# Optimization experiments

Hardware: AMD Instinct MI355X
Metric: run time of the kernel (lower is better)

## Reference

```python
import jax, jax.numpy as jnp
import numpy as np

N_NODES = 100000


def _gcn_norm(edge_index, num_nodes):
    # PyG GCNConv default: add self-loops, symmetric normalization.
    src = jnp.concatenate([edge_index[0], jnp.arange(num_nodes, dtype=edge_index.dtype)])
    dst = jnp.concatenate([edge_index[1], jnp.arange(num_nodes, dtype=edge_index.dtype)])
    deg = jax.ops.segment_sum(jnp.ones_like(dst, dtype=jnp.float32), dst, num_segments=num_nodes)
    dis = jnp.where(deg > 0, jax.lax.rsqrt(deg), 0.0)  # deg^{-1/2}
    norm = dis[src] * dis[dst]  # [E + N]
    return src, dst, norm


def _gcn_conv(x, W, b, src, dst, norm, num_nodes):
    h = x @ W.T                      # [N, out] transform first (out < in)
    msg = h[src] * norm[:, None]     # gather + per-edge scale
    agg = jax.ops.segment_sum(msg, dst, num_segments=num_nodes)  # scatter-add
    return agg + b


def setup_inputs() -> dict:
    key = jax.random.key(0)
    ks = jax.random.split(key, 12)
    E = 3200000
    x = jax.random.normal(ks[0], (N_NODES, 128), dtype=jnp.float32)
    edge_index = jax.random.randint(ks[1], (2, E), 0, N_NODES, dtype=jnp.int64)
    s = lambda k, sh, fan: jax.random.normal(k, sh, dtype=jnp.float32) * (1.0 / np.sqrt(fan))
    return {
        "x": x,
        "edge_index": edge_index,
        "W1": s(ks[2], (32, 128), 128), "b1": jnp.zeros((32,), jnp.float32),
        "W2": s(ks[3], (16, 32), 32),   "b2": jnp.zeros((16,), jnp.float32),
        "w_ih": s(ks[4], (32, 16), 16), "w_hh": s(ks[5], (32, 8), 8),
        "b_ih": s(ks[6], (32,), 8),     "b_hh": s(ks[7], (32,), 8),
        "W_out": s(ks[8], (1, 8), 8),   "b_out": jnp.zeros((1,), jnp.float32),
    }


def reference(x, edge_index, W1, b1, W2, b2, w_ih, w_hh, b_ih, b_hh, W_out, b_out):
    src, dst, norm = _gcn_norm(edge_index, N_NODES)
    h = jax.nn.relu(_gcn_conv(x, W1, b1, src, dst, norm, N_NODES))   # [N, 32]
    h = jax.nn.relu(_gcn_conv(h, W2, b2, src, dst, norm, N_NODES))   # [N, 16]
    # Single-timestep LSTM with h0 = c0 = 0 (gate order: i, f, g, o).
    gates = h @ w_ih.T + b_ih + b_hh   # [N, 32]; h0 @ w_hh.T term is zero
    i, f, g, o = jnp.split(gates, 4, axis=-1)
    c = jax.nn.sigmoid(i) * jnp.tanh(g)
    hh = jax.nn.sigmoid(o) * jnp.tanh(c)  # [N, 8]
    out = hh @ W_out.T + b_out            # [N, 1]
    return out.squeeze(-1)                # [N]
```

## Files before the change

### kernel.cpp

```cpp
#include <hip/hip_runtime.h>
#include <hip/hip_fp16.h>
#include <math.h>

static constexpr int N = 100000;
static constexpr int SHIFT = 7;
static constexpr int BUCKN = 1 << SHIFT;
static constexpr int NBUCK = (N + BUCKN - 1) >> SHIFT;
static constexpr int CHUNK = 12288;
static constexpr int STRIDE = 5120;

__global__ __launch_bounds__(1024) void k_init(int* __restrict__ gcur) {
    int b = threadIdx.x;
    if (b < NBUCK) gcur[b] = b * STRIDE;
}

__global__ __launch_bounds__(1024) void k_part(const int* __restrict__ src,
                                               const int* __restrict__ dst,
                                               int* __restrict__ gcur,
                                               int* __restrict__ col, int E) {
    __shared__ int ss[CHUNK];
    __shared__ int ds[CHUNK];
    __shared__ int hl[NBUCK];
    __shared__ int cur[NBUCK];
    const int t = threadIdx.x, b = blockIdx.x;
    if (t < NBUCK) hl[t] = 0;
    __syncthreads();
    const int e0 = b * CHUNK;
    const int m = min(CHUNK, E - e0);
    for (int i = t; i < m; i += 1024) {
        int d = dst[e0 + i], s = src[e0 + i];
        ss[i] = s;
        ds[i] = d;
        atomicAdd(&hl[d >> SHIFT], 1);
    }
    __syncthreads();
    if (t < NBUCK) cur[t] = atomicAdd(&gcur[t], hl[t]);
    __syncthreads();
    for (int i = t; i < m; i += 1024) {
        int d = ds[i];
        int pos = atomicAdd(&cur[d >> SHIFT], 1);
        col[pos] = ss[i] | ((d & (BUCKN - 1)) << 17);
    }
}

__global__ __launch_bounds__(1024) void k_sort(const int* __restrict__ gcur,
                                               int* __restrict__ col,
                                               int* __restrict__ deg,
                                               int* __restrict__ row_start) {
    __shared__ int es[STRIDE];
    __shared__ int cnt[BUCKN];
    __shared__ int cur[BUCKN];
    const int t = threadIdx.x, buck = blockIdx.x;
    const int s0 = buck * STRIDE;
    int n = gcur[buck] - s0;
    if (n > STRIDE) n = STRIDE;
    if (t < BUCKN) cnt[t] = 0;
    __syncthreads();
    for (int i = t; i < n; i += 1024) {
        int p = col[s0 + i];
        es[i] = p;
        atomicAdd(&cnt[(p >> 17) & (BUCKN - 1)], 1);
    }
    __syncthreads();
    if (t < BUCKN) cur[t] = cnt[t];
    __syncthreads();
    for (int off = 1; off < BUCKN; off <<= 1) {
        int v = (t < BUCKN && t >= off) ? cur[t - off] : 0;
        __syncthreads();
        if (t < BUCKN) cur[t] += v;
        __syncthreads();
    }
    if (t < BUCKN) {
        int excl = cur[t] - cnt[t];
        int node = buck * BUCKN + t;
        if (node < N) {
            deg[node] = cnt[t];
            row_start[node] = s0 + excl;
        }
        cur[t] = excl;
    }
    __syncthreads();
    for (int i = t; i < n; i += 1024) {
        int p = es[i];
        int pos = atomicAdd(&cur[(p >> 17) & (BUCKN - 1)], 1);
        col[s0 + pos] = p & 0x1FFFF;
    }
}

__global__ __launch_bounds__(256) void k_xw1(
        const float* __restrict__ x, const float* __restrict__ W1,
        const int* __restrict__ deg, __half* __restrict__ g1h) {
    __shared__ float wt[128 * 33];
    __shared__ float xs[8 * 128];
    const int t = threadIdx.x;
    for (int idx = t; idx < 4096; idx += 256) {
        int j = idx >> 7, k = idx & 127;
        wt[k * 33 + j] = W1[idx];
    }
    const float4* x4 = (const float4*)x + (size_t)blockIdx.x * 256;
    ((float4*)xs)[t] = x4[t];
    __syncthreads();

    const int nl = t >> 5, j = t & 31;
    const int node = blockIdx.x * 8 + nl;
    const float* xr = xs + nl * 128;
    float a = 0.f;
#pragma unroll 8
    for (int k = 0; k < 128; ++k) a = fmaf(xr[k], wt[k * 33 + j], a);
    g1h[blockIdx.x * 256 + t] = __float2half(a * rsqrtf((float)(deg[node] + 1)));
}

__global__ __launch_bounds__(256) void k_gather1(
        const int* __restrict__ row_start, const int* __restrict__ deg,
        const int* __restrict__ col, const __half* __restrict__ g1h,
        const float* __restrict__ b1, float* __restrict__ h1) {
    const int t = threadIdx.x;
    const int node = blockIdx.x * 8 + (t >> 5);
    const int j = t & 31;
    const int rs = row_start[node];
    const int ne = deg[node];
    float s0 = __half2float(g1h[node * 32 + j]), s1 = 0.f, s2 = 0.f, s3 = 0.f;
    for (int base = 0; base < ne; base += 32) {
        const int e = base + j;
        const int sv = (e < ne) ? col[rs + e] : 0;
        const int rem = ne - base;
#pragma unroll
        for (int k = 0; k < 32; k += 4) {
            int i0 = __shfl(sv, k + 0, 32);
            int i1 = __shfl(sv, k + 1, 32);
            int i2 = __shfl(sv, k + 2, 32);
            int i3 = __shfl(sv, k + 3, 32);
            float w0 = (k + 0 < rem) ? 1.f : 0.f;
            float w1 = (k + 1 < rem) ? 1.f : 0.f;
            float w2 = (k + 2 < rem) ? 1.f : 0.f;
            float w3 = (k + 3 < rem) ? 1.f : 0.f;
            s0 = fmaf(w0, __half2float(g1h[i0 * 32 + j]), s0);
            s1 = fmaf(w1, __half2float(g1h[i1 * 32 + j]), s1);
            s2 = fmaf(w2, __half2float(g1h[i2 * 32 + j]), s2);
            s3 = fmaf(w3, __half2float(g1h[i3 * 32 + j]), s3);
        }
    }
    float sum = (s0 + s1) + (s2 + s3);
    float v = sum * rsqrtf((float)(ne + 1)) + b1[j];
    h1[node * 32 + j] = v > 0.f ? v : 0.f;
}

__global__ __launch_bounds__(256) void k_layer2(
        const float* __restrict__ h1, const float* __restrict__ W2,
        const int* __restrict__ deg, __half* __restrict__ g2h) {
    __shared__ float h1s[16 * 32];
    __shared__ float w2t[32 * 17];
    const int t = threadIdx.x;
    for (int idx = t; idx < 512; idx += 256) {
        int j = idx >> 5, k = idx & 31;
        w2t[k * 17 + j] = W2[idx];
    }
    const int base = blockIdx.x * 512;
    for (int idx = t; idx < 512; idx += 256) h1s[idx] = h1[base + idx];
    __syncthreads();
    const int nl = t >> 4, j = t & 15;
    const int node = blockIdx.x * 16 + nl;
    const float* hr = h1s + nl * 32;
    float a = 0.f;
#pragma unroll
    for (int k = 0; k < 32; ++k) a = fmaf(hr[k], w2t[k * 17 + j], a);
    g2h[blockIdx.x * 256 + t] = __float2half(a * rsqrtf((float)(deg[node] + 1)));
}

__global__ __launch_bounds__(256) void k_gather2(
        const int* __restrict__ row_start, const int* __restrict__ deg,
        const int* __restrict__ col, const __half* __restrict__ g2h,
        const float* __restrict__ b2, float* __restrict__ h2) {
    const int t = threadIdx.x;
    const int node = blockIdx.x * 16 + (t >> 4);
    const int j = t & 15;
    const int rs = row_start[node];
    const int ne = deg[node];
    float s0 = __half2float(g2h[node * 16 + j]), s1 = 0.f, s2 = 0.f, s3 = 0.f;
    for (int base = 0; base < ne; base += 16) {
        const int e = base + j;
        const int sv = (e < ne) ? col[rs + e] : 0;
        const int rem = ne - base;
#pragma unroll
        for (int k = 0; k < 16; k += 4) {
            int i0 = __shfl(sv, k + 0, 16);
            int i1 = __shfl(sv, k + 1, 16);
            int i2 = __shfl(sv, k + 2, 16);
            int i3 = __shfl(sv, k + 3, 16);
            float w0 = (k + 0 < rem) ? 1.f : 0.f;
            float w1 = (k + 1 < rem) ? 1.f : 0.f;
            float w2 = (k + 2 < rem) ? 1.f : 0.f;
            float w3 = (k + 3 < rem) ? 1.f : 0.f;
            s0 = fmaf(w0, __half2float(g2h[i0 * 16 + j]), s0);
            s1 = fmaf(w1, __half2float(g2h[i1 * 16 + j]), s1);
            s2 = fmaf(w2, __half2float(g2h[i2 * 16 + j]), s2);
            s3 = fmaf(w3, __half2float(g2h[i3 * 16 + j]), s3);
        }
    }
    float sum = (s0 + s1) + (s2 + s3);
    float v = sum * rsqrtf((float)(ne + 1)) + b2[j];
    h2[node * 16 + j] = v > 0.f ? v : 0.f;
}

__global__ __launch_bounds__(256) void k_final(
        const float* __restrict__ h2g,
        const float* __restrict__ w_ih, const float* __restrict__ b_ih,
        const float* __restrict__ b_hh, const float* __restrict__ W_out,
        const float* __restrict__ b_out, float* __restrict__ out) {
    __shared__ float wih[512];
    __shared__ float bias[32];
    __shared__ float wout[8];
    __shared__ float bo;
    const int t = threadIdx.x;
    for (int idx = t; idx < 512; idx += 256) wih[idx] = w_ih[idx];
    if (t < 32) bias[t] = b_ih[t] + b_hh[t];
    if (t < 8)  wout[t] = W_out[t];
    if (t == 0) bo = b_out[0];
    __syncthreads();

    const int i = blockIdx.x * 256 + t;
    if (i >= N) return;
    float h2[16];
    const float4* a4 = (const float4*)(h2g + (size_t)i * 16);
#pragma unroll
    for (int q = 0; q < 4; ++q) {
        float4 v = a4[q];
        h2[q * 4 + 0] = v.x; h2[q * 4 + 1] = v.y;
        h2[q * 4 + 2] = v.z; h2[q * 4 + 3] = v.w;
    }
    float oacc = 0.f;
#pragma unroll
    for (int q = 0; q < 8; ++q) {
        float gi = bias[q], gg = bias[16 + q], go = bias[24 + q];
#pragma unroll
        for (int k = 0; k < 16; ++k) {
            gi = fmaf(h2[k], wih[q * 16 + k], gi);
            gg = fmaf(h2[k], wih[(16 + q) * 16 + k], gg);
            go = fmaf(h2[k], wih[(24 + q) * 16 + k], go);
        }
        float c  = (1.f / (1.f + expf(-gi))) * tanhf(gg);
        float hh = (1.f / (1.f + expf(-go))) * tanhf(c);
        oacc = fmaf(hh, wout[q], oacc);
    }
    out[i] = oacc + bo;
}

extern "C" void kernel_launch(void* const* d_in, const int* in_sizes, int n_in,
                              void* d_out, int out_size, void* d_ws, size_t ws_size,
                              hipStream_t stream) {
    const float* x     = (const float*)d_in[0];
    const int*   ei    = (const int*)d_in[1];
    const float* W1    = (const float*)d_in[2];
    const float* b1    = (const float*)d_in[3];
    const float* W2    = (const float*)d_in[4];
    const float* b2    = (const float*)d_in[5];
    const float* w_ih  = (const float*)d_in[6];
    const float* b_ih  = (const float*)d_in[8];
    const float* b_hh  = (const float*)d_in[9];
    const float* W_out = (const float*)d_in[10];
    const float* b_out = (const float*)d_in[11];
    float* out = (float*)d_out;

    const int E = in_sizes[1] / 2;
    const int* src = ei;
    const int* dst = ei + E;
    const int BP = (E + CHUNK - 1) / CHUNK;

    int* col       = (int*)d_ws;
    int* deg       = col + (size_t)NBUCK * STRIDE;
    int* row_start = deg + N;
    int* gcur      = row_start + N;
    __half* g1h    = (__half*)(gcur + 784);
    float* h1      = (float*)((int*)(gcur + 784) + (size_t)N * 16);
    __half* g2h    = g1h;
    float* h2      = h1;

    k_init   <<<1,               1024, 0, stream>>>(gcur);
    k_part   <<<BP,              1024, 0, stream>>>(src, dst, gcur, col, E);
    k_sort   <<<NBUCK,           1024, 0, stream>>>(gcur, col, deg, row_start);
    k_xw1    <<<N / 8,           256,  0, stream>>>(x, W1, deg, g1h);
    k_gather1<<<N / 8,           256,  0, stream>>>(row_start, deg, col, g1h, b1, h1);
    k_layer2 <<<N / 16,          256,  0, stream>>>(h1, W2, deg, g2h);
    k_gather2<<<N / 16,          256,  0, stream>>>(row_start, deg, col, g2h, b2, h2);
    k_final  <<<(N + 255) / 256, 256,  0, stream>>>(h2, w_ih, b_ih, b_hh, W_out, b_out, out);
}
```

Measured before the change: 286.2 us.

## Vectorize gather kernels with 16-byte row loads and register-block the x·W1 GEMM

The two neighbor-aggregation kernels now give each node a few lanes (4 for layer 1, 2 for layer 2). Each lane loads 8 fp16 features per neighbor as a uint4 and keeps 8 independent loads in flight, replacing the earlier one-half-per-lane scalar gathers. This is meant to cut the number of memory transactions and raise memory-level parallelism on the random-access gathers. The x·W1 kernel now uses float4 shared-memory tiles and has each thread compute 4 nodes, reusing the W1 values. Costs: more registers per thread, and fewer lanes per node, which could hurt nodes with high degree.

```diff
diff --git a/kernel.cpp b/kernel.cpp
--- a/kernel.cpp
+++ b/kernel.cpp
@@ -90,24 +90,37 @@
 __global__ __launch_bounds__(256) void k_xw1(
         const float* __restrict__ x, const float* __restrict__ W1,
         const int* __restrict__ deg, __half* __restrict__ g1h) {
-    __shared__ float wt[128 * 33];
-    __shared__ float xs[8 * 128];
-    const int t = threadIdx.x;
-    for (int idx = t; idx < 4096; idx += 256) {
-        int j = idx >> 7, k = idx & 127;
-        wt[k * 33 + j] = W1[idx];
-    }
-    const float4* x4 = (const float4*)x + (size_t)blockIdx.x * 256;
-    ((float4*)xs)[t] = x4[t];
-    __syncthreads();
-
-    const int nl = t >> 5, j = t & 31;
-    const int node = blockIdx.x * 8 + nl;
-    const float* xr = xs + nl * 128;
-    float a = 0.f;
-#pragma unroll 8
-    for (int k = 0; k < 128; ++k) a = fmaf(xr[k], wt[k * 33 + j], a);
-    g1h[blockIdx.x * 256 + t] = __float2half(a * rsqrtf((float)(deg[node] + 1)));
+    __shared__ float4 wtv[32 * 33];
+    __shared__ float4 xsv[1024];
+    const int t = threadIdx.x;
+    const float4* W1v = (const float4*)W1;
+    for (int idx = t; idx < 1024; idx += 256) {
+        int j = idx >> 5, kb = idx & 31;
+        wtv[kb * 33 + j] = W1v[idx];
+    }
+    const float4* x4 = (const float4*)x + (size_t)blockIdx.x * 1024;
+    for (int idx = t; idx < 1024; idx += 256) xsv[idx] = x4[idx];
+    __syncthreads();
+
+    const int j = t & 31, ng = t >> 5;
+    float a0 = 0.f, a1 = 0.f, a2 = 0.f, a3 = 0.f;
+#pragma unroll 4
+    for (int kb = 0; kb < 32; ++kb) {
+        float4 w = wtv[kb * 33 + j];
+        float4 x0 = xsv[(4 * ng + 0) * 32 + kb];
+        float4 x1 = xsv[(4 * ng + 1) * 32 + kb];
+        float4 x2 = xsv[(4 * ng + 2) * 32 + kb];
+        float4 x3 = xsv[(4 * ng + 3) * 32 + kb];
+        a0 = fmaf(w.x, x0.x, fmaf(w.y, x0.y, fmaf(w.z, x0.z, fmaf(w.w, x0.w, a0))));
+        a1 = fmaf(w.x, x1.x, fmaf(w.y, x1.y, fmaf(w.z, x1.z, fmaf(w.w, x1.w, a1))));
+        a2 = fmaf(w.x, x2.x, fmaf(w.y, x2.y, fmaf(w.z, x2.z, fmaf(w.w, x2.w, a2))));
+        a3 = fmaf(w.x, x3.x, fmaf(w.y, x3.y, fmaf(w.z, x3.z, fmaf(w.w, x3.w, a3))));
+    }
+    const int nb = blockIdx.x * 32 + 4 * ng;
+    g1h[(nb + 0) * 32 + j] = __float2half(a0 * rsqrtf((float)(deg[nb + 0] + 1)));
+    g1h[(nb + 1) * 32 + j] = __float2half(a1 * rsqrtf((float)(deg[nb + 1] + 1)));
+    g1h[(nb + 2) * 32 + j] = __float2half(a2 * rsqrtf((float)(deg[nb + 2] + 1)));
+    g1h[(nb + 3) * 32 + j] = __float2half(a3 * rsqrtf((float)(deg[nb + 3] + 1)));
 }
 
 __global__ __launch_bounds__(256) void k_gather1(
@@ -115,34 +128,65 @@
         const int* __restrict__ col, const __half* __restrict__ g1h,
         const float* __restrict__ b1, float* __restrict__ h1) {
     const int t = threadIdx.x;
-    const int node = blockIdx.x * 8 + (t >> 5);
-    const int j = t & 31;
-    const int rs = row_start[node];
-    const int ne = deg[node];
-    float s0 = __half2float(g1h[node * 32 + j]), s1 = 0.f, s2 = 0.f, s3 = 0.f;
-    for (int base = 0; base < ne; base += 32) {
-        const int e = base + j;
-        const int sv = (e < ne) ? col[rs + e] : 0;
-        const int rem = ne - base;
-#pragma unroll
-        for (int k = 0; k < 32; k += 4) {
-            int i0 = __shfl(sv, k + 0, 32);
-            int i1 = __shfl(sv, k + 1, 32);
-            int i2 = __shfl(sv, k + 2, 32);
-            int i3 = __shfl(sv, k + 3, 32);
-            float w0 = (k + 0 < rem) ? 1.f : 0.f;
-            float w1 = (k + 1 < rem) ? 1.f : 0.f;
-            float w2 = (k + 2 < rem) ? 1.f : 0.f;
-            float w3 = (k + 3 < rem) ? 1.f : 0.f;
-            s0 = fmaf(w0, __half2float(g1h[i0 * 32 + j]), s0);
-            s1 = fmaf(w1, __half2float(g1h[i1 * 32 + j]), s1);
-            s2 = fmaf(w2, __half2float(g1h[i2 * 32 + j]), s2);
-            s3 = fmaf(w3, __half2float(g1h[i3 * 32 + j]), s3);
-        }
-    }
-    float sum = (s0 + s1) + (s2 + s3);
-    float v = sum * rsqrtf((float)(ne + 1)) + b1[j];
-    h1[node * 32 + j] = v > 0.f ? v : 0.f;
+    const int lane = t & 63, w = t >> 6;
+    const int q = lane & 3;
+    const int node = blockIdx.x * 64 + w * 16 + (lane >> 2);
+    const int nc = node < N ? node : N - 1;
+    const int rs = row_start[nc];
+    const int ne = (node < N) ? deg[nc] : 0;
+    const uint4* g1v = (const uint4*)g1h;
+
+    float acc[8];
+    {
+        uint4 rv = g1v[nc * 4 + q];
+        const __half2* hp = (const __half2*)&rv;
+#pragma unroll
+        for (int m2 = 0; m2 < 4; ++m2) {
+            float2 f = __half22float2(hp[m2]);
+            acc[2 * m2] = f.x;
+            acc[2 * m2 + 1] = f.y;
+        }
+    }
+    for (int base = 0; base < ne; base += 8) {
+        int sva = (base + q < ne) ? col[rs + base + q] : 0;
+        int svb = (base + 4 + q < ne) ? col[rs + base + 4 + q] : 0;
+        int idx[8];
+#pragma unroll
+        for (int u = 0; u < 4; ++u) idx[u] = __shfl(sva, u, 4);
+#pragma unroll
+        for (int u = 0; u < 4; ++u) idx[4 + u] = __shfl(svb, u, 4);
+        uint4 rv[8];
+#pragma unroll
+        for (int u = 0; u < 8; ++u) rv[u] = g1v[idx[u] * 4 + q];
+#pragma unroll
+        for (int u = 0; u < 8; ++u) {
+            float wt = (base + u < ne) ? 1.f : 0.f;
+            const __half2* hp = (const __half2*)&rv[u];
+#pragma unroll
+            for (int m2 = 0; m2 < 4; ++m2) {
+                float2 f = __half22float2(hp[m2]);
+                acc[2 * m2]     = fmaf(wt, f.x, acc[2 * m2]);
+                acc[2 * m2 + 1] = fmaf(wt, f.y, acc[2 * m2 + 1]);
+            }
+        }
+    }
+    if (node < N) {
+        const float dis = rsqrtf((float)(ne + 1));
+        float4* h1v = (float4*)h1;
+#pragma unroll
+        for (int h = 0; h < 2; ++h) {
+            float4 o;
+            float v0 = acc[4 * h + 0] * dis + b1[q * 8 + 4 * h + 0];
+            float v1 = acc[4 * h + 1] * dis + b1[q * 8 + 4 * h + 1];
+            float v2 = acc[4 * h + 2] * dis + b1[q * 8 + 4 * h + 2];
+            float v3 = acc[4 * h + 3] * dis + b1[q * 8 + 4 * h + 3];
+            o.x = v0 > 0.f ? v0 : 0.f;
+            o.y = v1 > 0.f ? v1 : 0.f;
+            o.z = v2 > 0.f ? v2 : 0.f;
+            o.w = v3 > 0.f ? v3 : 0.f;
+            h1v[node * 8 + q * 2 + h] = o;
+        }
+    }
 }
 
 __global__ __launch_bounds__(256) void k_layer2(
@@ -172,34 +216,68 @@
         const int* __restrict__ col, const __half* __restrict__ g2h,
         const float* __restrict__ b2, float* __restrict__ h2) {
     const int t = threadIdx.x;
-    const int node = blockIdx.x * 16 + (t >> 4);
-    const int j = t & 15;
-    const int rs = row_start[node];
-    const int ne = deg[node];
-    float s0 = __half2float(g2h[node * 16 + j]), s1 = 0.f, s2 = 0.f, s3 = 0.f;
-    for (int base = 0; base < ne; base += 16) {
-        const int e = base + j;
-        const int sv = (e < ne) ? col[rs + e] : 0;
-        const int rem = ne - base;
-#pragma unroll
-        for (int k = 0; k < 16; k += 4) {
-            int i0 = __shfl(sv, k + 0, 16);
-            int i1 = __shfl(sv, k + 1, 16);
-            int i2 = __shfl(sv, k + 2, 16);
-            int i3 = __shfl(sv, k + 3, 16);
-            float w0 = (k + 0 < rem) ? 1.f : 0.f;
-            float w1 = (k + 1 < rem) ? 1.f : 0.f;
-            float w2 = (k + 2 < rem) ? 1.f : 0.f;
-            float w3 = (k + 3 < rem) ? 1.f : 0.f;
-            s0 = fmaf(w0, __half2float(g2h[i0 * 16 + j]), s0);
-            s1 = fmaf(w1, __half2float(g2h[i1 * 16 + j]), s1);
-            s2 = fmaf(w2, __half2float(g2h[i2 * 16 + j]), s2);
-            s3 = fmaf(w3, __half2float(g2h[i3 * 16 + j]), s3);
-        }
-    }
-    float sum = (s0 + s1) + (s2 + s3);
-    float v = sum * rsqrtf((float)(ne + 1)) + b2[j];
-    h2[node * 16 + j] = v > 0.f ? v : 0.f;
+    const int lane = t & 63, w = t >> 6;
+    const int q = lane & 1;
+    const int node = blockIdx.x * 128 + w * 32 + (lane >> 1);
+    const int nc = node < N ? node : N - 1;
+    const int rs = row_start[nc];
+    const int ne = (node < N) ? deg[nc] : 0;
+    const uint4* g2v = (const uint4*)g2h;
+
+    float acc[8];
+    {
+        uint4 rv = g2v[nc * 2 + q];
+        const __half2* hp = (const __half2*)&rv;
+#pragma unroll
+        for (int m2 = 0; m2 < 4; ++m2) {
+            float2 f = __half22float2(hp[m2]);
+            acc[2 * m2] = f.x;
+            acc[2 * m2 + 1] = f.y;
+        }
+    }
+    for (int base = 0; base < ne; base += 8) {
+        int sv[4];
+#pragma unroll
+        for (int k = 0; k < 4; ++k)
+            sv[k] = (base + 2 * k + q < ne) ? col[rs + base + 2 * k + q] : 0;
+        int idx[8];
+#pragma unroll
+        for (int k = 0; k < 4; ++k) {
+            idx[2 * k]     = __shfl(sv[k], 0, 2);
+            idx[2 * k + 1] = __shfl(sv[k], 1, 2);
+        }
+        uint4 rv[8];
+#pragma unroll
+        for (int u = 0; u < 8; ++u) rv[u] = g2v[idx[u] * 2 + q];
+#pragma unroll
+        for (int u = 0; u < 8; ++u) {
+            float wt = (base + u < ne) ? 1.f : 0.f;
+            const __half2* hp = (const __half2*)&rv[u];
+#pragma unroll
+            for (int m2 = 0; m2 < 4; ++m2) {
+                float2 f = __half22float2(hp[m2]);
+                acc[2 * m2]     = fmaf(wt, f.x, acc[2 * m2]);
+                acc[2 * m2 + 1] = fmaf(wt, f.y, acc[2 * m2 + 1]);
+            }
+        }
+    }
+    if (node < N) {
+        const float dis = rsqrtf((float)(ne + 1));
+        float4* h2v = (float4*)h2;
+#pragma unroll
+        for (int h = 0; h < 2; ++h) {
+            float4 o;
+            float v0 = acc[4 * h + 0] * dis + b2[q * 8 + 4 * h + 0];
+            float v1 = acc[4 * h + 1] * dis + b2[q * 8 + 4 * h + 1];
+            float v2 = acc[4 * h + 2] * dis + b2[q * 8 + 4 * h + 2];
+            float v3 = acc[4 * h + 3] * dis + b2[q * 8 + 4 * h + 3];
+            o.x = v0 > 0.f ? v0 : 0.f;
+            o.y = v1 > 0.f ? v1 : 0.f;
+            o.z = v2 > 0.f ? v2 : 0.f;
+            o.w = v3 > 0.f ? v3 : 0.f;
+            h2v[node * 4 + q * 2 + h] = o;
+        }
+    }
 }
 
 __global__ __launch_bounds__(256) void k_final(
@@ -275,12 +353,12 @@
     __half* g2h    = g1h;
     float* h2      = h1;
 
-    k_init   <<<1,               1024, 0, stream>>>(gcur);
-    k_part   <<<BP,              1024, 0, stream>>>(src, dst, gcur, col, E);
-    k_sort   <<<NBUCK,           1024, 0, stream>>>(gcur, col, deg, row_start);
-    k_xw1    <<<N / 8,           256,  0, stream>>>(x, W1, deg, g1h);
-    k_gather1<<<N / 8,           256,  0, stream>>>(row_start, deg, col, g1h, b1, h1);
-    k_layer2 <<<N / 16,          256,  0, stream>>>(h1, W2, deg, g2h);
-    k_gather2<<<N / 16,          256,  0, stream>>>(row_start, deg, col, g2h, b2, h2);
-    k_final  <<<(N + 255) / 256, 256,  0, stream>>>(h2, w_ih, b_ih, b_hh, W_out, b_out, out);
-}
+    k_init   <<<1,                      1024, 0, stream>>>(gcur);
+    k_part   <<<BP,                     1024, 0, stream>>>(src, dst, gcur, col, E);
+    k_sort   <<<NBUCK,                  1024, 0, stream>>>(gcur, col, deg, row_start);
+    k_xw1    <<<N / 32,                 256,  0, stream>>>(x, W1, deg, g1h);
+    k_gather1<<<(N + 63) / 64,          256,  0, stream>>>(row_start, deg, col, g1h, b1, h1);
+    k_layer2 <<<N / 16,                 256,  0, stream>>>(h1, W2, deg, g2h);
+    k_gather2<<<(N + 127) / 128,        256,  0, stream>>>(row_start, deg, col, g2h, b2, h2);
+    k_final  <<<(N + 255) / 256,        256,  0, stream>>>(h2, w_ih, b_ih, b_hh, W_out, b_out, out);
+}
```

Measured after the change: 279.1 us. 2.5% less time.
